# Optimization experiments

Measured on AMD Instinct MI355X. Metric: run time of the kernel, lower is better.

Reference implementation:

```python
import jax, jax.numpy as jnp
import numpy as np
from jax import lax

C = 256            # channels
K = 7              # kernel_size
RED = 4            # reduction_ratio
GC = 16            # group_channels
G = C // GC        # groups
PAD = (K - 1) // 2
EPS = 1e-5


def setup_inputs() -> dict:
    key = jax.random.key(0)
    ks = jax.random.split(key, 8)
    B, H, W = 4, 64, 64
    x = jax.random.normal(ks[0], (B, C, H, W), dtype=jnp.float32)
    # conv1: 1x1 conv C -> C/4, then BN (eval-mode running stats), ReLU
    w1 = jax.random.normal(ks[1], (C // RED, C), dtype=jnp.float32) * (1.0 / np.sqrt(C))
    b1 = jnp.zeros((C // RED,), dtype=jnp.float32)
    gamma = jnp.ones((C // RED,), dtype=jnp.float32)
    beta = jnp.zeros((C // RED,), dtype=jnp.float32)
    mean = jax.random.normal(ks[2], (C // RED,), dtype=jnp.float32) * 0.1
    var = jax.random.uniform(ks[3], (C // RED,), dtype=jnp.float32, minval=0.5, maxval=1.5)
    # conv2: 1x1 conv C/4 -> K^2 * G
    w2 = jax.random.normal(ks[4], (K * K * G, C // RED), dtype=jnp.float32) * (1.0 / np.sqrt(C // RED))
    b2 = jnp.zeros((K * K * G,), dtype=jnp.float32)
    return {"x": x, "w1": w1, "b1": b1, "gamma": gamma, "beta": beta,
            "mean": mean, "var": var, "w2": w2, "b2": b2}


def reference(x, w1, b1, gamma, beta, mean, var, w2, b2):
    b, c, h, w = x.shape
    # kernel-generation branch (stride==1, so no avgpool)
    t = jnp.einsum('bchw,oc->bohw', x, w1) + b1[None, :, None, None]
    t = gamma[None, :, None, None] * (t - mean[None, :, None, None]) \
        * lax.rsqrt(var + EPS)[None, :, None, None] + beta[None, :, None, None]
    t = jax.nn.relu(t)
    weight = jnp.einsum('bchw,oc->bohw', t, w2) + b2[None, :, None, None]
    # (b, G, 1, K*K, h, w)
    weight = weight.reshape(b, G, K * K, h, w)[:, :, None]
    # im2col patches: (b, C*K*K, h, w) with channel-major (c, kh, kw) ordering,
    # matching torch.nn.Unfold
    patches = lax.conv_general_dilated_patches(
        x, filter_shape=(K, K), window_strides=(1, 1),
        padding=((PAD, PAD), (PAD, PAD)))
    patches = patches.reshape(b, G, GC, K * K, h, w)
    out = (weight * patches).sum(axis=3).reshape(b, C, h, w)
    return out
```

## Files before the change

### kernel.cpp

```cpp
#include <hip/hip_runtime.h>

#define C_IN 256
#define CR   64
#define G_   16
#define GC_  16
#define K_   7
#define KK   49
#define PAD_ 3
#define H_   64
#define W_   64
#define HW   4096
#define OO   784
#define EPSV 1e-5f
#define WTAPS 13

__global__ __launch_bounds__(256) void prep_kernel(
    const float* __restrict__ w1, const float* __restrict__ b1,
    const float* __restrict__ gamma, const float* __restrict__ beta,
    const float* __restrict__ mean, const float* __restrict__ var,
    const float* __restrict__ w2,
    float* __restrict__ w1t, float* __restrict__ b1f, float* __restrict__ w2t)
{
  int idx = blockIdx.x * 256 + threadIdx.x;
  if (idx < CR * C_IN) {
    int o = idx / C_IN, c = idx % C_IN;
    float s = gamma[o] * rsqrtf(var[o] + EPSV);
    w1t[c * CR + o] = w1[idx] * s;
  }
  if (idx < CR) {
    float s = gamma[idx] * rsqrtf(var[idx] + EPSV);
    b1f[idx] = (b1[idx] - mean[idx]) * s + beta[idx];
  }
  if (idx < OO * CR) {
    int o = idx / CR, c = idx % CR;
    w2t[c * OO + o] = w2[idx];
  }
}

__global__ __launch_bounds__(256) void conv1_kernel(
    const float* __restrict__ x, const float* __restrict__ w1t,
    const float* __restrict__ b1f, float* __restrict__ t)
{
  const int quad = threadIdx.x & 15;
  const int oi   = threadIdx.x >> 4;
  const int o0   = blockIdx.y * 32 + oi * 2;
  const int hw0  = blockIdx.x * 64 + quad * 4;
  const int b    = blockIdx.z;

  const float* xb = x + ((size_t)b * C_IN) * HW + hw0;

  float acc0[4] = {0.f, 0.f, 0.f, 0.f};
  float acc1[4] = {0.f, 0.f, 0.f, 0.f};

  for (int c = 0; c < C_IN; ++c) {
    float xv[4];
    *(float4*)xv = *(const float4*)(xb + (size_t)c * HW);
    const float w0v = w1t[c * CR + o0];
    const float w1v = w1t[c * CR + o0 + 1];
#pragma unroll
    for (int p = 0; p < 4; ++p) {
      acc0[p] = fmaf(xv[p], w0v, acc0[p]);
      acc1[p] = fmaf(xv[p], w1v, acc1[p]);
    }
  }

  const float bb0 = b1f[o0], bb1 = b1f[o0 + 1];
  float r0[4], r1[4];
#pragma unroll
  for (int p = 0; p < 4; ++p) {
    r0[p] = fmaxf(acc0[p] + bb0, 0.f);
    r1[p] = fmaxf(acc1[p] + bb1, 0.f);
  }
  float* tb = t + ((size_t)b * CR) * HW + hw0;
  *(float4*)(tb + (size_t)o0 * HW)       = *(float4*)r0;
  *(float4*)(tb + (size_t)(o0 + 1) * HW) = *(float4*)r1;
}

__global__ __launch_bounds__(256) void conv2invol_kernel(
    const float* __restrict__ x, const float* __restrict__ t,
    const float* __restrict__ w2t,
    const float* __restrict__ b2, float* __restrict__ out)
{
  __shared__ float wlds[KK * 64];
  const int tid = threadIdx.x;
  const int row = blockIdx.x;
  const int g   = blockIdx.y;
  const int b   = blockIdx.z;

  {
    const int px  = tid & 63;
    const int j   = __builtin_amdgcn_readfirstlane(tid >> 6);
    const int kk0 = j * WTAPS;

    float acc[WTAPS];
#pragma unroll
    for (int i = 0; i < WTAPS; ++i) {
      int kk = kk0 + i;
      acc[i] = (kk < KK) ? b2[g * KK + kk] : 0.f;
    }

    const float* tb  = t + ((size_t)b * CR) * HW + row * W_ + px;
    const float* w2g = w2t + g * KK;
    for (int c = 0; c < CR; ++c) {
      float xv = tb[(size_t)c * HW];
      const int base = c * OO;
#pragma unroll
      for (int i = 0; i < WTAPS; ++i) {
        int kk = kk0 + i; kk = kk < KK ? kk : KK - 1;
        acc[i] = fmaf(xv, w2g[base + kk], acc[i]);
      }
    }
#pragma unroll
    for (int i = 0; i < WTAPS; ++i) {
      int kk = kk0 + i;
      if (kk < KK) wlds[kk * 64 + px] = acc[i];
    }
  }
  __syncthreads();

  const int quad = tid & 15;
  const int gc   = tid >> 4;
  const int w0   = quad * 4;

  float acc4[4] = {0.f, 0.f, 0.f, 0.f};
  const float* xp = x + ((size_t)b * C_IN + g * GC_ + gc) * HW;

#pragma unroll
  for (int kh = 0; kh < K_; ++kh) {
    const int y = row + kh - PAD_;
    if ((unsigned)y < (unsigned)H_) {
      const float* xr = xp + y * W_;
      float win[12];
      float4 zero4 = {0.f, 0.f, 0.f, 0.f};
      *(float4*)&win[0] = (w0 >= 4)  ? *(const float4*)(xr + w0 - 4) : zero4;
      *(float4*)&win[4] = *(const float4*)(xr + w0);
      *(float4*)&win[8] = (w0 <= 56) ? *(const float4*)(xr + w0 + 4) : zero4;
#pragma unroll
      for (int dw = 0; dw < 7; ++dw) {
        float wv[4];
        *(float4*)wv = *(const float4*)&wlds[(kh * 7 + dw) * 64 + w0];
#pragma unroll
        for (int cc = 0; cc < 4; ++cc)
          acc4[cc] = fmaf(wv[cc], win[cc + dw + 1], acc4[cc]);
      }
    }
  }

  float* ob = out + ((size_t)b * C_IN + g * GC_ + gc) * HW + row * W_ + w0;
  *(float4*)ob = *(float4*)acc4;
}

extern "C" void kernel_launch(void* const* d_in, const int* in_sizes, int n_in,
                              void* d_out, int out_size, void* d_ws, size_t ws_size,
                              hipStream_t stream) {
  const float* x     = (const float*)d_in[0];
  const float* w1    = (const float*)d_in[1];
  const float* b1    = (const float*)d_in[2];
  const float* gamma = (const float*)d_in[3];
  const float* beta  = (const float*)d_in[4];
  const float* mean  = (const float*)d_in[5];
  const float* var   = (const float*)d_in[6];
  const float* w2    = (const float*)d_in[7];
  const float* b2    = (const float*)d_in[8];
  float* out = (float*)d_out;
  const int B = in_sizes[0] / (C_IN * HW);

  char* p = (char*)d_ws;
  float* w1t = (float*)p;  p += ((size_t)CR * C_IN * 4 + 255) & ~(size_t)255;
  float* b1f = (float*)p;  p += ((size_t)CR * 4 + 255) & ~(size_t)255;
  float* w2t = (float*)p;  p += ((size_t)OO * CR * 4 + 511) & ~(size_t)255;
  float* t   = (float*)p;

  prep_kernel<<<dim3((OO * CR + 255) / 256), 256, 0, stream>>>(
      w1, b1, gamma, beta, mean, var, w2, w1t, b1f, w2t);

  conv1_kernel<<<dim3(HW / 64, 2, B), 256, 0, stream>>>(x, w1t, b1f, t);

  conv2invol_kernel<<<dim3(H_, G_, B), 256, 0, stream>>>(x, t, w2t, b2, out);
}
```

Baseline: 189.9 us.

## Store conv1 output pixel-major and remap involution blocks across XCDs

conv1 now writes the intermediate t in a pixel-major (HW, CR) layout. Each 1024-thread block covers 64 pixels across all 64 output channels, so x is read once per pixel tile instead of twice. The involution kernel reads t with float4 loads along channels. Its 1D grid is remapped so that blocks running on the same XCD share batch, row and group neighbourhoods, which is meant to improve L2 reuse. The t stores in conv1 are now strided by 256 bytes per lane, which risks poorly coalesced writes.

```diff
diff --git a/kernel.cpp b/kernel.cpp
--- a/kernel.cpp
+++ b/kernel.cpp
@@ -37,43 +37,36 @@
   }
 }
 
-__global__ __launch_bounds__(256) void conv1_kernel(
+__global__ __launch_bounds__(1024) void conv1_kernel(
     const float* __restrict__ x, const float* __restrict__ w1t,
     const float* __restrict__ b1f, float* __restrict__ t)
 {
-  const int quad = threadIdx.x & 15;
-  const int oi   = threadIdx.x >> 4;
-  const int o0   = blockIdx.y * 32 + oi * 2;
-  const int hw0  = blockIdx.x * 64 + quad * 4;
-  const int b    = blockIdx.z;
+  const int px = threadIdx.x & 63;
+  const int j  = __builtin_amdgcn_readfirstlane(threadIdx.x >> 6);
+  const int o0 = j * 4;
+  const int hw0 = blockIdx.x * 64;
+  const int b   = blockIdx.y;
 
-  const float* xb = x + ((size_t)b * C_IN) * HW + hw0;
+  const float* xb = x + ((size_t)b * C_IN) * HW + hw0 + px;
 
-  float acc0[4] = {0.f, 0.f, 0.f, 0.f};
-  float acc1[4] = {0.f, 0.f, 0.f, 0.f};
-
+  float acc[4] = {0.f, 0.f, 0.f, 0.f};
+#pragma unroll 8
   for (int c = 0; c < C_IN; ++c) {
-    float xv[4];
-    *(float4*)xv = *(const float4*)(xb + (size_t)c * HW);
-    const float w0v = w1t[c * CR + o0];
-    const float w1v = w1t[c * CR + o0 + 1];
-#pragma unroll
-    for (int p = 0; p < 4; ++p) {
-      acc0[p] = fmaf(xv[p], w0v, acc0[p]);
-      acc1[p] = fmaf(xv[p], w1v, acc1[p]);
-    }
+    float xv = xb[(size_t)c * HW];
+    float4 wv = *(const float4*)(w1t + c * CR + o0);
+    acc[0] = fmaf(xv, wv.x, acc[0]);
+    acc[1] = fmaf(xv, wv.y, acc[1]);
+    acc[2] = fmaf(xv, wv.z, acc[2]);
+    acc[3] = fmaf(xv, wv.w, acc[3]);
   }
 
-  const float bb0 = b1f[o0], bb1 = b1f[o0 + 1];
-  float r0[4], r1[4];
-#pragma unroll
-  for (int p = 0; p < 4; ++p) {
-    r0[p] = fmaxf(acc0[p] + bb0, 0.f);
-    r1[p] = fmaxf(acc1[p] + bb1, 0.f);
-  }
-  float* tb = t + ((size_t)b * CR) * HW + hw0;
-  *(float4*)(tb + (size_t)o0 * HW)       = *(float4*)r0;
-  *(float4*)(tb + (size_t)(o0 + 1) * HW) = *(float4*)r1;
+  float4 bb = *(const float4*)(b1f + o0);
+  float r[4];
+  r[0] = fmaxf(acc[0] + bb.x, 0.f);
+  r[1] = fmaxf(acc[1] + bb.y, 0.f);
+  r[2] = fmaxf(acc[2] + bb.z, 0.f);
+  r[3] = fmaxf(acc[3] + bb.w, 0.f);
+  *(float4*)(t + ((size_t)(b * HW + hw0 + px)) * CR + o0) = *(float4*)r;
 }
 
 __global__ __launch_bounds__(256) void conv2invol_kernel(
@@ -83,9 +76,14 @@
 {
   __shared__ float wlds[KK * 64];
   const int tid = threadIdx.x;
-  const int row = blockIdx.x;
-  const int g   = blockIdx.y;
-  const int b   = blockIdx.z;
+
+  const int L     = blockIdx.x;
+  const int xcd   = L & 7;
+  const int chunk = L >> 3;
+  const int g     = chunk >> 5;
+  const int pr    = (chunk & 31) + (xcd << 5);
+  const int b     = pr >> 6;
+  const int row   = pr & 63;
 
   {
     const int px  = tid & 63;
@@ -95,19 +93,23 @@
     float acc[WTAPS];
 #pragma unroll
     for (int i = 0; i < WTAPS; ++i) {
-      int kk = kk0 + i;
-      acc[i] = (kk < KK) ? b2[g * KK + kk] : 0.f;
+      int kk = kk0 + i; kk = kk < KK ? kk : KK - 1;
+      acc[i] = b2[g * KK + kk];
     }
 
-    const float* tb  = t + ((size_t)b * CR) * HW + row * W_ + px;
-    const float* w2g = w2t + g * KK;
-    for (int c = 0; c < CR; ++c) {
-      float xv = tb[(size_t)c * HW];
-      const int base = c * OO;
+    const float* tb = t + ((size_t)(b * HW + row * W_ + px)) * CR;
+#pragma unroll 4
+    for (int c0 = 0; c0 < 16; ++c0) {
+      float xv[4];
+      *(float4*)xv = *(const float4*)(tb + 4 * c0);
 #pragma unroll
-      for (int i = 0; i < WTAPS; ++i) {
-        int kk = kk0 + i; kk = kk < KK ? kk : KK - 1;
-        acc[i] = fmaf(xv, w2g[base + kk], acc[i]);
+      for (int cc = 0; cc < 4; ++cc) {
+        const float* wr = w2t + (4 * c0 + cc) * OO + g * KK;
+#pragma unroll
+        for (int i = 0; i < WTAPS; ++i) {
+          int kk = kk0 + i; kk = kk < KK ? kk : KK - 1;
+          acc[i] = fmaf(xv[cc], wr[kk], acc[i]);
+        }
       }
     }
 #pragma unroll
@@ -174,7 +176,7 @@
   prep_kernel<<<dim3((OO * CR + 255) / 256), 256, 0, stream>>>(
       w1, b1, gamma, beta, mean, var, w2, w1t, b1f, w2t);
 
-  conv1_kernel<<<dim3(HW / 64, 2, B), 256, 0, stream>>>(x, w1t, b1f, t);
+  conv1_kernel<<<dim3(HW / 64, B), 1024, 0, stream>>>(x, w1t, b1f, t);
 
-  conv2invol_kernel<<<dim3(H_, G_, B), 256, 0, stream>>>(x, t, w2t, b2, out);
+  conv2invol_kernel<<<dim3(H_ * G_ * B), 256, 0, stream>>>(x, t, w2t, b2, out);
 }
```

Result: faster. 180.2 us (-5.1%).
